# Kernel tuning notes

Hardware: AMD Instinct MI355X
Metric: run time of the kernel (lower is better)

## Reference

```python
import jax, jax.numpy as jnp
import numpy as np

B, L, D, H, FF = 2, 4096, 512, 8, 2048
HD = D // H
EPS = 1e-5


def _layer_norm(x, g, b):
    mu = jnp.mean(x, axis=-1, keepdims=True)
    var = jnp.mean(jnp.square(x - mu), axis=-1, keepdims=True)
    return (x - mu) * jax.lax.rsqrt(var + EPS) * g + b


def setup_inputs() -> dict:
    key = jax.random.key(0)
    ks = jax.random.split(key, 16)
    s = 1.0 / np.sqrt(D)
    inp = {
        'x': jax.random.normal(ks[0], (B, L, D), dtype=jnp.float32),
        'Wq': jax.random.normal(ks[1], (D, D), dtype=jnp.float32) * s,
        'bq': jnp.zeros((D,), jnp.float32),
        'Wk': jax.random.normal(ks[2], (D, D), dtype=jnp.float32) * s,
        'bk': jnp.zeros((D,), jnp.float32),
        'Wv': jax.random.normal(ks[3], (D, D), dtype=jnp.float32) * s,
        'bv': jnp.zeros((D,), jnp.float32),
        'Wo': jax.random.normal(ks[4], (D, D), dtype=jnp.float32) * s,
        'bo': jnp.zeros((D,), jnp.float32),
        'ln1_g': jnp.ones((D,), jnp.float32),
        'ln1_b': jnp.zeros((D,), jnp.float32),
        'W1': jax.random.normal(ks[5], (D, FF), dtype=jnp.float32) * s,
        'b1': jnp.zeros((FF,), jnp.float32),
        'W2': jax.random.normal(ks[6], (FF, D), dtype=jnp.float32) * (1.0 / np.sqrt(FF)),
        'b2': jnp.zeros((D,), jnp.float32),
        'ln2_g': jnp.ones((D,), jnp.float32),
        'ln2_b': jnp.zeros((D,), jnp.float32),
        'window': 128,
    }
    return inp


def reference(x, Wq, bq, Wk, bk, Wv, bv, Wo, bo, ln1_g, ln1_b, W1, b1, W2, b2, ln2_g, ln2_b, window):
    # ---- local (banded) self-attention, matching nn.MultiheadAttention math ----
    q = (x @ Wq + bq).reshape(B, L, H, HD)
    k = (x @ Wk + bk).reshape(B, L, H, HD)
    v = (x @ Wv + bv).reshape(B, L, H, HD)
    scale = 1.0 / np.sqrt(HD)
    scores = jnp.einsum('bqhd,bkhd->bhqk', q, k) * scale  # [B,H,L,L]
    idx = jnp.arange(L)
    band = jnp.abs(idx[None, :] - idx[:, None]) > window   # True = masked
    scores = jnp.where(band[None, None], -jnp.inf, scores)
    probs = jax.nn.softmax(scores, axis=-1)
    attn = jnp.einsum('bhqk,bkhd->bqhd', probs, v).reshape(B, L, D)
    attn = attn @ Wo + bo
    # ---- residual + norm1 ----
    h = _layer_norm(x + attn, ln1_g, ln1_b)
    # ---- FFN + residual + norm2 (dropout=0 at eval) ----
    ff = jax.nn.relu(h @ W1 + b1) @ W2 + b2
    return _layer_norm(h + ff, ln2_g, ln2_b)
```

## Files before the change

### kernel.cpp

```cpp
#include <hip/hip_runtime.h>

namespace {

constexpr int B = 2, L = 4096, D = 512, H = 8, FF = 2048;
constexpr int M = B * L;
constexpr float LN_EPS = 1e-5f;

typedef __attribute__((ext_vector_type(8))) short short8;
typedef __attribute__((ext_vector_type(4))) float floatx4;

typedef __attribute__((address_space(3))) unsigned int lds_uint;
typedef const __attribute__((address_space(1))) unsigned int glob_uint;

__device__ __forceinline__ void gl_lds16(const unsigned short* g, unsigned short* l) {
  __builtin_amdgcn_global_load_lds((glob_uint*)g, (lds_uint*)l, 16, 0, 0);
}

__device__ __forceinline__ unsigned short f2bf(float f) {
  union { float f; unsigned u; } v; v.f = f;
  unsigned r = v.u + 0x7FFFu + ((v.u >> 16) & 1u);
  return (unsigned short)(r >> 16);
}

__device__ __forceinline__ float bf2f(unsigned short b) {
  union { unsigned u; float f; } v; v.u = ((unsigned)b) << 16;
  return v.f;
}

__global__ __launch_bounds__(256)
void k_prep(const float* __restrict__ x,
            const float* __restrict__ Wq, const float* __restrict__ Wk,
            const float* __restrict__ Wv, const float* __restrict__ Wo,
            const float* __restrict__ W1, const float* __restrict__ W2,
            const float* __restrict__ bq, const float* __restrict__ bk,
            const float* __restrict__ bv,
            unsigned short* __restrict__ Xb,
            unsigned short* __restrict__ WqkvT, unsigned short* __restrict__ WoT,
            unsigned short* __restrict__ W1T, unsigned short* __restrict__ W2T,
            float* __restrict__ bqkv) {
  __shared__ unsigned short tile[64 * 72];
  if (blockIdx.x < 4102) {
    int tid = blockIdx.x * blockDim.x + threadIdx.x;
    if (tid < 1048576) {
      float4 v = ((const float4*)x)[tid];
      ((ushort4*)Xb)[tid] = make_ushort4(f2bf(v.x), f2bf(v.y), f2bf(v.z), f2bf(v.w));
      return;
    }
    int u = tid - 1048576;
    if (u < 1536) bqkv[u] = (u < 512) ? bq[u] : (u < 1024 ? bk[u - 512] : bv[u - 1024]);
    return;
  }
  const int t = blockIdx.x - 4102;
  const float* src; unsigned short* dst; int Ns, Kd, n0, k0, nsrc0;
  if (t < 192) {
    int nt = t % 24, kt = t / 24; int ng = nt * 64;
    src = ng < 512 ? Wq : (ng < 1024 ? Wk : Wv);
    Ns = 512; Kd = 512; n0 = ng; nsrc0 = ng & 511; k0 = kt * 64; dst = WqkvT;
  } else if (t < 256) {
    int u = t - 192; int nt = u % 8, kt = u / 8;
    src = Wo; Ns = 512; Kd = 512; n0 = nt * 64; nsrc0 = n0; k0 = kt * 64; dst = WoT;
  } else if (t < 512) {
    int u = t - 256; int nt = u % 32, kt = u / 32;
    src = W1; Ns = 2048; Kd = 512; n0 = nt * 64; nsrc0 = n0; k0 = kt * 64; dst = W1T;
  } else {
    int u = t - 512; int nt = u % 8, kt = u / 8;
    src = W2; Ns = 512; Kd = 2048; n0 = nt * 64; nsrc0 = n0; k0 = kt * 64; dst = W2T;
  }
  const int tid = threadIdx.x;
  {
    int r = tid >> 2, cs = (tid & 3) * 16;
    const float4* sp = (const float4*)(src + (size_t)(k0 + r) * Ns + nsrc0 + cs);
    unsigned short* tp = &tile[r * 72 + cs];
#pragma unroll
    for (int i = 0; i < 4; ++i) {
      float4 v = sp[i];
      tp[i * 4 + 0] = f2bf(v.x); tp[i * 4 + 1] = f2bf(v.y);
      tp[i * 4 + 2] = f2bf(v.z); tp[i * 4 + 3] = f2bf(v.w);
    }
  }
  __syncthreads();
  {
    int n = tid >> 2, ks = (tid & 3) * 16;
    unsigned short buf[16];
#pragma unroll
    for (int e = 0; e < 16; ++e) buf[e] = tile[(ks + e) * 72 + n];
    unsigned short* dp = dst + (size_t)(n0 + n) * Kd + k0 + ks;
    *(short8*)dp = *(const short8*)&buf[0];
    *(short8*)(dp + 8) = *(const short8*)&buf[8];
  }
}

template <int EPI>
__global__ __launch_bounds__(256, 3)
void k_gemm(const unsigned short* __restrict__ A, const unsigned short* __restrict__ BT,
            const float* __restrict__ bias, void* __restrict__ Cout,
            unsigned short* __restrict__ Vout,
            const int klen, const int N) {
  __shared__ unsigned short lA[2][128 * 32];
  __shared__ unsigned short lB[2][128 * 32];
  const int tid = threadIdx.x;
  const int wave = tid >> 6, lane = tid & 63;
  const int quad = lane >> 4, l16 = lane & 15;
  const int m0 = blockIdx.y * 128, n0 = blockIdx.x * 128;
  const int wm = (wave >> 1) * 64, wn = (wave & 1) * 64;
  const int kbeg = blockIdx.z * klen;
  const size_t Kdim = (size_t)klen * gridDim.z;

  const floatx4 fzero = {0.f, 0.f, 0.f, 0.f};
  floatx4 acc[4][4];
#pragma unroll
  for (int i = 0; i < 4; ++i)
#pragma unroll
    for (int j = 0; j < 4; ++j) acc[i][j] = fzero;

  const int r0 = tid >> 2, o0 = (tid & 3) * 8;
  const int r1 = (256 + tid) >> 2, o1 = (tid & 3) * 8;
  const unsigned short* Ag0 = A + (size_t)(m0 + r0) * Kdim + kbeg + o0;
  const unsigned short* Ag1 = A + (size_t)(m0 + r1) * Kdim + kbeg + o1;
  const unsigned short* Bg0 = BT + (size_t)(n0 + r0) * Kdim + kbeg + o0;
  const unsigned short* Bg1 = BT + (size_t)(n0 + r1) * Kdim + kbeg + o1;

  auto stage = [&](int buf, int kt) {
    gl_lds16(Ag0 + kt, &lA[buf][wave * 512]);
    gl_lds16(Ag1 + kt, &lA[buf][(4 + wave) * 512]);
    gl_lds16(Bg0 + kt, &lB[buf][wave * 512]);
    gl_lds16(Bg1 + kt, &lB[buf][(4 + wave) * 512]);
  };

  stage(0, 0);
  __syncthreads();

  int buf = 0;
  for (int kt = 0; kt < klen; kt += 32, buf ^= 1) {
    if (kt + 32 < klen) stage(buf ^ 1, kt + 32);
    short8 af[4], bf[4];
#pragma unroll
    for (int i = 0; i < 4; ++i)
      af[i] = *(const short8*)&lA[buf][(wm + i * 16 + l16) * 32 + quad * 8];
#pragma unroll
    for (int j = 0; j < 4; ++j)
      bf[j] = *(const short8*)&lB[buf][(wn + j * 16 + l16) * 32 + quad * 8];
#pragma unroll
    for (int i = 0; i < 4; ++i)
#pragma unroll
      for (int j = 0; j < 4; ++j)
        acc[i][j] = __builtin_amdgcn_mfma_f32_16x16x32_bf16(af[i], bf[j], acc[i][j], 0, 0, 0);
    __syncthreads();
  }

  float* outf = (float*)Cout + (size_t)blockIdx.z * M * N;
  const bool vblock = (EPI == 3) && (n0 >= 1024);
#pragma unroll
  for (int j = 0; j < 4; ++j) {
    const int col = n0 + wn + j * 16 + l16;
    const float bv = (blockIdx.z == 0) ? bias[col] : 0.f;
#pragma unroll
    for (int i = 0; i < 4; ++i) {
      const int row = m0 + wm + i * 16 + quad * 4;
      if (EPI == 3 && vblock) {
        const int hh = (col - 1024) >> 6, dd = (col - 1024) & 63;
        const int bb = row >> 12, keyl = row & 4095;
        ushort4 pk = make_ushort4(f2bf(acc[i][j][0] + bv), f2bf(acc[i][j][1] + bv),
                                  f2bf(acc[i][j][2] + bv), f2bf(acc[i][j][3] + bv));
        *(ushort4*)(Vout + ((size_t)(bb * 8 + hh) * 64 + dd) * L + keyl) = pk;
      } else {
#pragma unroll
        for (int r = 0; r < 4; ++r) {
          float v = acc[i][j][r] + bv;
          if (EPI == 1) v = fmaxf(v, 0.f);
          if (EPI == 2)
            outf[(size_t)(row + r) * N + col] = v;
          else
            ((unsigned short*)Cout)[(size_t)(row + r) * N + col] = f2bf(v);
        }
      }
    }
  }
}

__global__ __launch_bounds__(256, 4)
void k_attn(const unsigned short* __restrict__ QKV, const unsigned short* __restrict__ Vg,
            unsigned short* __restrict__ attnb, const int* __restrict__ wptr) {
  const int W = wptr[0];
  __shared__ unsigned short Kt[2][4096];
  __shared__ unsigned short Vt[2][4096];
  const int tid = threadIdx.x;
  const int wave = tid >> 6, lane = tid & 63;
  const int quad = lane >> 4, l16 = lane & 15;
  const int blk = blockIdx.x;
  const int qt = blk & 63, h = (blk >> 6) & 7, b = blk >> 9;
  const int q0blk = qt * 64;
  const int q0 = q0blk + wave * 16;
  const float scale = 0.125f;

  const unsigned short* Kbase = QKV + (size_t)(b * L) * 1536 + 512 + h * 64;
  const unsigned short* Vh = Vg + (size_t)(b * 8 + h) * 64 * L;

  auto stage = [&](int buf, int jbg) {
#pragma unroll
    for (int i = 0; i < 2; ++i) {
      int c = i * 256 + tid;
      int kr = c >> 3;
      int key = jbg + kr;
      int keyc = key < 0 ? 0 : (key > L - 1 ? L - 1 : key);
      int dpart = (c & 7) ^ (kr & 7) ^ (((kr >> 3) & 3) << 1);
      gl_lds16(Kbase + (size_t)keyc * 1536 + dpart * 8,
               &Kt[buf][(i * 256 + wave * 64) * 8]);
    }
#pragma unroll
    for (int i = 0; i < 2; ++i) {
      int c = i * 256 + tid;
      int d = c >> 3;
      int kpart = (c & 7) ^ (d & 7);
      int kb = jbg + kpart * 8;
      kb = kb < 0 ? 0 : (kb > L - 8 ? L - 8 : kb);
      gl_lds16(Vh + (size_t)d * L + kb,
               &Vt[buf][(i * 256 + wave * 64) * 8]);
    }
  };

  const unsigned short* Qp = QKV + (size_t)(b * L + q0 + l16) * 1536 + h * 64;
  short8 qf0 = *(const short8*)(Qp + quad * 8);
  short8 qf1 = *(const short8*)(Qp + 32 + quad * 8);

  int koff[4][2];
#pragma unroll
  for (int tt = 0; tt < 4; ++tt) {
    int krow = (tt >> 1) * 32 + ((l16 >> 2) << 3) + (tt & 1) * 4 + (l16 & 3);
    int s2 = (krow & 7) ^ (((krow >> 3) & 3) << 1);
    koff[tt][0] = (krow * 8 + (quad ^ s2)) * 8;
    koff[tt][1] = (krow * 8 + ((quad + 4) ^ s2)) * 8;
  }
  int voff[4][2];
#pragma unroll
  for (int nt = 0; nt < 4; ++nt) {
    int d = nt * 16 + l16;
    voff[nt][0] = (d * 8 + (quad ^ (d & 7))) * 8;
    voff[nt][1] = (d * 8 + ((quad + 4) ^ (d & 7))) * 8;
  }

  const floatx4 fzero = {0.f, 0.f, 0.f, 0.f};
  floatx4 o[4];
#pragma unroll
  for (int i = 0; i < 4; ++i) o[i] = fzero;
  float lsum = 0.f;
  const int q = q0 + l16;

  stage(0, q0blk - 128);
  __syncthreads();

  for (int it = 0; it < 5; ++it) {
    const int jbg = q0blk - 128 + it * 64;
    if (it < 4) stage((it + 1) & 1, jbg + 64);
    const unsigned short* lk = Kt[it & 1];
    const unsigned short* lv = Vt[it & 1];
    unsigned pu[8];
#pragma unroll
    for (int tt = 0; tt < 4; ++tt) {
      const short8 kf0 = *(const short8*)&lk[koff[tt][0]];
      const short8 kf1 = *(const short8*)&lk[koff[tt][1]];
      floatx4 z = fzero;
      z = __builtin_amdgcn_mfma_f32_16x16x32_bf16(kf0, qf0, z, 0, 0, 0);
      z = __builtin_amdgcn_mfma_f32_16x16x32_bf16(kf1, qf1, z, 0, 0, 0);
      const int kb0 = jbg + (tt >> 1) * 32 + quad * 8 + (tt & 1) * 4;
      float pv[4];
#pragma unroll
      for (int r = 0; r < 4; ++r) {
        int key = kb0 + r;
        int dd = q - key; dd = dd < 0 ? -dd : dd;
        bool ok = (key >= 0) && (key < L) && (dd <= W);
        float p = ok ? __expf(z[r] * scale) : 0.f;
        lsum += p;
        pv[r] = p;
      }
      pu[tt * 2 + 0] = (unsigned)f2bf(pv[0]) | ((unsigned)f2bf(pv[1]) << 16);
      pu[tt * 2 + 1] = (unsigned)f2bf(pv[2]) | ((unsigned)f2bf(pv[3]) << 16);
    }
    union { unsigned u[4]; short8 v; } pa0, pa1;
    pa0.u[0] = pu[0]; pa0.u[1] = pu[1]; pa0.u[2] = pu[2]; pa0.u[3] = pu[3];
    pa1.u[0] = pu[4]; pa1.u[1] = pu[5]; pa1.u[2] = pu[6]; pa1.u[3] = pu[7];
#pragma unroll
    for (int nt = 0; nt < 4; ++nt) {
      const short8 vf0 = *(const short8*)&lv[voff[nt][0]];
      const short8 vf1 = *(const short8*)&lv[voff[nt][1]];
      o[nt] = __builtin_amdgcn_mfma_f32_16x16x32_bf16(pa0.v, vf0, o[nt], 0, 0, 0);
      o[nt] = __builtin_amdgcn_mfma_f32_16x16x32_bf16(pa1.v, vf1, o[nt], 0, 0, 0);
    }
    __syncthreads();
  }
  lsum += __shfl_xor(lsum, 16, 64);
  lsum += __shfl_xor(lsum, 32, 64);
#pragma unroll
  for (int r = 0; r < 4; ++r) {
    float inv = 1.f / __shfl(lsum, quad * 4 + r, 64);
    size_t base = (size_t)(b * L + q0 + quad * 4 + r) * 512 + h * 64;
#pragma unroll
    for (int nt = 0; nt < 4; ++nt)
      attnb[base + nt * 16 + l16] = f2bf(o[nt][r] * inv);
  }
}

template <int RESBF>
__global__ __launch_bounds__(256, 2)
void k_res_ln(const float* __restrict__ t0, const float* __restrict__ t1,
              const void* __restrict__ res,
              const float* __restrict__ gamma, const float* __restrict__ beta,
              float* __restrict__ outf, unsigned short* __restrict__ outb) {
  const int wave = threadIdx.x >> 6, lane = threadIdx.x & 63;
  const int row = blockIdx.x * 4 + wave;
  const float4* tv = (const float4*)(t0 + (size_t)row * D);
  float4 a0 = tv[lane], a1 = tv[lane + 64];
  float4 b0, b1;
  if (RESBF) {
    const ushort4* rv = (const ushort4*)((const unsigned short*)res + (size_t)row * D);
    ushort4 u0 = rv[lane], u1 = rv[lane + 64];
    b0 = make_float4(bf2f(u0.x), bf2f(u0.y), bf2f(u0.z), bf2f(u0.w));
    b1 = make_float4(bf2f(u1.x), bf2f(u1.y), bf2f(u1.z), bf2f(u1.w));
  } else {
    const float4* rv = (const float4*)((const float*)res + (size_t)row * D);
    b0 = rv[lane]; b1 = rv[lane + 64];
  }
  float4 y0 = make_float4(a0.x + b0.x, a0.y + b0.y, a0.z + b0.z, a0.w + b0.w);
  float4 y1 = make_float4(a1.x + b1.x, a1.y + b1.y, a1.z + b1.z, a1.w + b1.w);
  {
    const float4* uv = (const float4*)(t1 + (size_t)row * D);
    float4 c0 = uv[lane], c1 = uv[lane + 64];
    y0.x += c0.x; y0.y += c0.y; y0.z += c0.z; y0.w += c0.w;
    y1.x += c1.x; y1.y += c1.y; y1.z += c1.z; y1.w += c1.w;
  }
  float s = y0.x + y0.y + y0.z + y0.w + y1.x + y1.y + y1.z + y1.w;
  float q = y0.x * y0.x + y0.y * y0.y + y0.z * y0.z + y0.w * y0.w +
            y1.x * y1.x + y1.y * y1.y + y1.z * y1.z + y1.w * y1.w;
#pragma unroll
  for (int d = 1; d < 64; d <<= 1) {
    s += __shfl_xor(s, d, 64);
    q += __shfl_xor(q, d, 64);
  }
  const float mean = s * (1.f / D);
  const float var = q * (1.f / D) - mean * mean;
  const float rstd = rsqrtf(var + LN_EPS);
  float4 g0 = ((const float4*)gamma)[lane], g1 = ((const float4*)gamma)[lane + 64];
  float4 e0 = ((const float4*)beta)[lane], e1 = ((const float4*)beta)[lane + 64];
  float4 o0 = make_float4((y0.x - mean) * rstd * g0.x + e0.x, (y0.y - mean) * rstd * g0.y + e0.y,
                          (y0.z - mean) * rstd * g0.z + e0.z, (y0.w - mean) * rstd * g0.w + e0.w);
  float4 o1 = make_float4((y1.x - mean) * rstd * g1.x + e1.x, (y1.y - mean) * rstd * g1.y + e1.y,
                          (y1.z - mean) * rstd * g1.z + e1.z, (y1.w - mean) * rstd * g1.w + e1.w);
  if (outf) {
    ((float4*)(outf + (size_t)row * D))[lane] = o0;
    ((float4*)(outf + (size_t)row * D))[lane + 64] = o1;
  }
  if (outb) {
    ((ushort4*)(outb + (size_t)row * D))[lane] =
        make_ushort4(f2bf(o0.x), f2bf(o0.y), f2bf(o0.z), f2bf(o0.w));
    ((ushort4*)(outb + (size_t)row * D))[lane + 64] =
        make_ushort4(f2bf(o1.x), f2bf(o1.y), f2bf(o1.z), f2bf(o1.w));
  }
}

}

extern "C" void kernel_launch(void* const* d_in, const int* in_sizes, int n_in,
                              void* d_out, int out_size, void* d_ws, size_t ws_size,
                              hipStream_t stream) {
  const float* x   = (const float*)d_in[0];
  const float* Wq  = (const float*)d_in[1];
  const float* bq  = (const float*)d_in[2];
  const float* Wk  = (const float*)d_in[3];
  const float* bk  = (const float*)d_in[4];
  const float* Wv  = (const float*)d_in[5];
  const float* bv  = (const float*)d_in[6];
  const float* Wo  = (const float*)d_in[7];
  const float* bo  = (const float*)d_in[8];
  const float* g1  = (const float*)d_in[9];
  const float* be1 = (const float*)d_in[10];
  const float* W1  = (const float*)d_in[11];
  const float* b1  = (const float*)d_in[12];
  const float* W2  = (const float*)d_in[13];
  const float* b2  = (const float*)d_in[14];
  const float* g2  = (const float*)d_in[15];
  const float* be2 = (const float*)d_in[16];
  const int* wptr  = (const int*)d_in[17];
  float* out = (float*)d_out;

  char* w = (char*)d_ws;
  size_t off = 0;
  auto take = [&](size_t bytes) -> void* {
    void* p = w + off;
    off += (bytes + 255) & ~(size_t)255;
    return p;
  };
  unsigned short* Xb    = (unsigned short*)take((size_t)M * D * 2);
  unsigned short* QKVb  = (unsigned short*)take((size_t)M * 1536 * 2);
  unsigned short* attnb = (unsigned short*)take((size_t)M * D * 2);
  unsigned short* Vg    = (unsigned short*)take((size_t)M * D * 2);
  unsigned short* WqkvT = (unsigned short*)take((size_t)1536 * 512 * 2);
  unsigned short* WoT   = (unsigned short*)take((size_t)512 * 512 * 2);
  unsigned short* W1T   = (unsigned short*)take((size_t)2048 * 512 * 2);
  unsigned short* W2T   = (unsigned short*)take((size_t)512 * 2048 * 2);
  float* bqkv           = (float*)take(1536 * 4);
  float* tbuf           = (float*)take((size_t)2 * M * D * 4);
  unsigned short* hb    = (unsigned short*)take((size_t)M * D * 2);
  unsigned short* ffb   = (unsigned short*)take((size_t)M * FF * 2);

  k_prep<<<4870, 256, 0, stream>>>(x, Wq, Wk, Wv, Wo, W1, W2, bq, bk, bv,
                                   Xb, WqkvT, WoT, W1T, W2T, bqkv);
  k_gemm<3><<<dim3(12, 64, 1), 256, 0, stream>>>(Xb, WqkvT, bqkv, QKVb, Vg, 512, 1536);
  k_attn<<<B * H * (L / 64), 256, 0, stream>>>(QKVb, Vg, attnb, wptr);
  k_gemm<2><<<dim3(4, 64, 2), 256, 0, stream>>>(attnb, WoT, bo, tbuf, nullptr, 256, 512);
  k_res_ln<0><<<M / 4, 256, 0, stream>>>(tbuf, tbuf + (size_t)M * D, x, g1, be1, nullptr, hb);
  k_gemm<1><<<dim3(16, 64, 1), 256, 0, stream>>>(hb, W1T, b1, ffb, nullptr, 512, 2048);
  k_gemm<2><<<dim3(4, 64, 2), 256, 0, stream>>>(ffb, W2T, b2, tbuf, nullptr, 1024, 512);
  k_res_ln<1><<<M / 4, 256, 0, stream>>>(tbuf, tbuf + (size_t)M * D, hb, g2, be2, out, nullptr);
}
```

Before: 246.5 us.

## Remap blocks across XCDs, add unmasked attention fast path, use hardware bf16 pack

```diff
diff --git a/kernel.cpp b/kernel.cpp
--- a/kernel.cpp
+++ b/kernel.cpp
@@ -98,12 +98,20 @@
             const int klen, const int N) {
   __shared__ unsigned short lA[2][128 * 32];
   __shared__ unsigned short lB[2][128 * 32];
+  unsigned flat = blockIdx.x + gridDim.x * (blockIdx.y + gridDim.y * blockIdx.z);
+  const unsigned chunk = (gridDim.x * gridDim.y * gridDim.z) >> 3;
+  flat = (flat & 7) * chunk + (flat >> 3);
+  const unsigned bx = flat % gridDim.x;
+  const unsigned rest = flat / gridDim.x;
+  const unsigned by = rest % gridDim.y;
+  const unsigned bz = rest / gridDim.y;
+
   const int tid = threadIdx.x;
   const int wave = tid >> 6, lane = tid & 63;
   const int quad = lane >> 4, l16 = lane & 15;
-  const int m0 = blockIdx.y * 128, n0 = blockIdx.x * 128;
+  const int m0 = by * 128, n0 = bx * 128;
   const int wm = (wave >> 1) * 64, wn = (wave & 1) * 64;
-  const int kbeg = blockIdx.z * klen;
+  const int kbeg = bz * klen;
   const size_t Kdim = (size_t)klen * gridDim.z;
 
   const floatx4 fzero = {0.f, 0.f, 0.f, 0.f};
@@ -148,12 +156,12 @@
     __syncthreads();
   }
 
-  float* outf = (float*)Cout + (size_t)blockIdx.z * M * N;
+  float* outf = (float*)Cout + (size_t)bz * M * N;
   const bool vblock = (EPI == 3) && (n0 >= 1024);
 #pragma unroll
   for (int j = 0; j < 4; ++j) {
     const int col = n0 + wn + j * 16 + l16;
-    const float bv = (blockIdx.z == 0) ? bias[col] : 0.f;
+    const float bv = (bz == 0) ? bias[col] : 0.f;
 #pragma unroll
     for (int i = 0; i < 4; ++i) {
       const int row = m0 + wm + i * 16 + quad * 4;
@@ -187,8 +195,8 @@
   const int tid = threadIdx.x;
   const int wave = tid >> 6, lane = tid & 63;
   const int quad = lane >> 4, l16 = lane & 15;
-  const int blk = blockIdx.x;
-  const int qt = blk & 63, h = (blk >> 6) & 7, b = blk >> 9;
+  const int bid = (int)((blockIdx.x & 7) * (gridDim.x >> 3) + (blockIdx.x >> 3));
+  const int qt = bid & 63, h = (bid >> 6) & 7, b = bid >> 9;
   const int q0blk = qt * 64;
   const int q0 = q0blk + wave * 16;
   const float scale = 0.125f;
@@ -254,6 +262,8 @@
     if (it < 4) stage((it + 1) & 1, jbg + 64);
     const unsigned short* lk = Kt[it & 1];
     const unsigned short* lv = Vt[it & 1];
+    const int dhi = q0 + 15 - jbg, dlo = jbg + 63 - q0;
+    const bool fast = (jbg >= 0) && (jbg + 64 <= L) && ((dhi > dlo ? dhi : dlo) <= W);
     unsigned pu[8];
 #pragma unroll
     for (int tt = 0; tt < 4; ++tt) {
@@ -262,19 +272,31 @@
       floatx4 z = fzero;
       z = __builtin_amdgcn_mfma_f32_16x16x32_bf16(kf0, qf0, z, 0, 0, 0);
       z = __builtin_amdgcn_mfma_f32_16x16x32_bf16(kf1, qf1, z, 0, 0, 0);
-      const int kb0 = jbg + (tt >> 1) * 32 + quad * 8 + (tt & 1) * 4;
       float pv[4];
-#pragma unroll
-      for (int r = 0; r < 4; ++r) {
-        int key = kb0 + r;
-        int dd = q - key; dd = dd < 0 ? -dd : dd;
-        bool ok = (key >= 0) && (key < L) && (dd <= W);
-        float p = ok ? __expf(z[r] * scale) : 0.f;
-        lsum += p;
-        pv[r] = p;
+      if (fast) {
+#pragma unroll
+        for (int r = 0; r < 4; ++r) {
+          float p = __expf(z[r] * scale);
+          lsum += p;
+          pv[r] = p;
+        }
+      } else {
+        const int kb0 = jbg + (tt >> 1) * 32 + quad * 8 + (tt & 1) * 4;
+#pragma unroll
+        for (int r = 0; r < 4; ++r) {
+          int key = kb0 + r;
+          int dd = q - key; dd = dd < 0 ? -dd : dd;
+          bool okk = (key >= 0) && (key < L) && (dd <= W);
+          float p = okk ? __expf(z[r] * scale) : 0.f;
+          lsum += p;
+          pv[r] = p;
+        }
       }
-      pu[tt * 2 + 0] = (unsigned)f2bf(pv[0]) | ((unsigned)f2bf(pv[1]) << 16);
-      pu[tt * 2 + 1] = (unsigned)f2bf(pv[2]) | ((unsigned)f2bf(pv[3]) << 16);
+      unsigned lo, hi;
+      asm("v_cvt_pk_bf16_f32 %0, %1, %2" : "=v"(lo) : "v"(pv[0]), "v"(pv[1]));
+      asm("v_cvt_pk_bf16_f32 %0, %1, %2" : "=v"(hi) : "v"(pv[2]), "v"(pv[3]));
+      pu[tt * 2 + 0] = lo;
+      pu[tt * 2 + 1] = hi;
     }
     union { unsigned u[4]; short8 v; } pa0, pa1;
     pa0.u[0] = pu[0]; pa0.u[1] = pu[1]; pa0.u[2] = pu[2]; pa0.u[3] = pu[3];
```

New measurement: 233.7 us. 5.2% less time.
